# Kernel tuning notes

Measured on AMD Instinct MI355X. Metric: run time of the kernel, lower is better.

## Reference

```python
import jax, jax.numpy as jnp
import numpy as np

DIM = 512
HEADS = 8
SEQ = 2048
BATCH = 4


def setup_inputs() -> dict:
    key = jax.random.key(0)
    k = jax.random.split(key, 6)
    x = jax.random.normal(k[0], (BATCH, SEQ, DIM), dtype=jnp.float32)
    mask = jax.random.normal(k[1], (BATCH, SEQ, SEQ), dtype=jnp.float32)
    Wqkv = jax.random.normal(k[2], (3 * DIM, DIM), dtype=jnp.float32) * 0.02
    Btab = jax.random.normal(k[3], (1, HEADS, 2 * SEQ - 1), dtype=jnp.float32) * 0.02
    Wproj = jax.random.normal(k[4], (DIM, DIM), dtype=jnp.float32) * 0.02
    bproj = jax.random.normal(k[5], (DIM,), dtype=jnp.float32) * 0.02
    return {"x": x, "mask": mask, "Wqkv": Wqkv, "Btab": Btab,
            "Wproj": Wproj, "bproj": bproj}


def reference(x, mask, Wqkv, Btab, Wproj, bproj):
    B, N, C = x.shape
    H = Btab.shape[1]
    seq = (Btab.shape[2] + 1) // 2
    head_dim = C // H
    scale = head_dim ** (-0.5)

    # qkv projection (no bias), split into q,k,v of shape [B,H,N,head_dim]
    qkv = (x @ Wqkv.T).reshape(B, N, 3, H, head_dim)
    qkv = jnp.transpose(qkv, (2, 0, 3, 1, 4))  # [3,B,H,N,hd]
    q, k, v = qkv[0], qkv[1], qkv[2]

    # gathered relative-position bias: B_index[i,j] = i - j + seq - 1
    idx = jnp.arange(N)[:, None] - jnp.arange(N)[None, :] + (seq - 1)  # [N,N]
    bias = Btab[:, :, idx]  # [1,H,N,N]

    attn = jnp.einsum('bhnd,bhmd->bhnm', q, k) * scale + bias
    attn = attn + mask[:, None, :, :]  # additive mask, broadcast over heads
    attn = jax.nn.softmax(attn, axis=-1)

    out = jnp.einsum('bhnm,bhmd->bhnd', attn, v)  # [B,H,N,hd]
    out = jnp.transpose(out, (0, 2, 1, 3)).reshape(B, N, C)
    return out @ Wproj.T + bproj
```

## Files before the change

### kernel.cpp

```cpp
#include <hip/hip_runtime.h>


typedef __attribute__((ext_vector_type(8))) short short8;
typedef __attribute__((ext_vector_type(4))) float f32x4;

#define SEQ   2048
#define NHEAD 8
#define NBATCH 4
#define HD    64
#define CDIM  512
#define L2E   1.44269504f

__device__ __forceinline__ unsigned short f32_to_bf16_rn(float f) {
  unsigned u = __builtin_bit_cast(unsigned, f);
  u += 0x7FFFu + ((u >> 16) & 1u);
  return (unsigned short)(u >> 16);
}

__global__ __launch_bounds__(256) void cvt_f32_bf16(const float* __restrict__ in,
                                                    ushort* __restrict__ out, int n4) {
  int i = blockIdx.x * 256 + threadIdx.x;
  const int stride = gridDim.x * 256;
  for (; i < n4; i += stride) {
    float4 v = reinterpret_cast<const float4*>(in)[i];
    ushort4 o;
    o.x = f32_to_bf16_rn(v.x);
    o.y = f32_to_bf16_rn(v.y);
    o.z = f32_to_bf16_rn(v.z);
    o.w = f32_to_bf16_rn(v.w);
    reinterpret_cast<ushort4*>(out)[i] = o;
  }
}

template <int MODE>
__global__ __launch_bounds__(256) void gemm_nt(
    const ushort* __restrict__ A, const ushort* __restrict__ Bm,
    ushort* __restrict__ qo, ushort* __restrict__ ko, ushort* __restrict__ vto,
    const float* __restrict__ bias, float* __restrict__ outf) {
  const int K = 512;
  __shared__ ushort As[128 * 40];
  __shared__ ushort Bs[128 * 40];

  const int t = threadIdx.x;
  const int bn = blockIdx.x, bm = blockIdx.y;
  const int lane = t & 63, w = t >> 6;
  const int wm = w >> 1, wn = w & 1;
  const int lr = lane & 15, lq = lane >> 4;
  const int m0 = bm * 128, n0 = bn * 128;

  f32x4 acc[4][4];
#pragma unroll
  for (int i = 0; i < 4; ++i)
#pragma unroll
    for (int j = 0; j < 4; ++j) acc[i][j] = (f32x4){0.f, 0.f, 0.f, 0.f};

  for (int kt = 0; kt < K; kt += 32) {
#pragma unroll
    for (int p = 0; p < 2; ++p) {
      const int flat = p * 256 + t;
      const int row = flat >> 2, seg = flat & 3;
      *(uint4*)&As[row * 40 + seg * 8] =
          *(const uint4*)(A + (size_t)(m0 + row) * K + kt + seg * 8);
      *(uint4*)&Bs[row * 40 + seg * 8] =
          *(const uint4*)(Bm + (size_t)(n0 + row) * K + kt + seg * 8);
    }
    __syncthreads();

    short8 af[4], bf[4];
#pragma unroll
    for (int i = 0; i < 4; ++i) {
      af[i] = *(const short8*)&As[(wm * 64 + i * 16 + lr) * 40 + lq * 8];
      bf[i] = *(const short8*)&Bs[(wn * 64 + i * 16 + lr) * 40 + lq * 8];
    }
#pragma unroll
    for (int i = 0; i < 4; ++i)
#pragma unroll
      for (int j = 0; j < 4; ++j)
        acc[i][j] = __builtin_amdgcn_mfma_f32_16x16x32_bf16(af[i], bf[j], acc[i][j], 0, 0, 0);
    __syncthreads();
  }

  if constexpr (MODE == 0) {
#pragma unroll
    for (int i = 0; i < 4; ++i) {
      const int mbase = m0 + wm * 64 + i * 16 + lq * 4;
      const int bb = mbase >> 11;
      const int s0 = mbase & 2047;
#pragma unroll
      for (int j = 0; j < 4; ++j) {
        const int nb = n0 + wn * 64 + j * 16;
        const int tt = nb >> 9;
        const int hh = (nb >> 6) & 7;
        const int d0 = nb & 63;
        const int bh = bb * NHEAD + hh;
        if (tt == 2) {
          ushort4 pk;
          pk.x = f32_to_bf16_rn(acc[i][j][0]);
          pk.y = f32_to_bf16_rn(acc[i][j][1]);
          pk.z = f32_to_bf16_rn(acc[i][j][2]);
          pk.w = f32_to_bf16_rn(acc[i][j][3]);
          *(ushort4*)(vto + ((size_t)bh * HD + d0 + lr) * SEQ + s0) = pk;
        } else {
          ushort* dst = (tt == 0) ? qo : ko;
#pragma unroll
          for (int r = 0; r < 4; ++r)
            dst[((size_t)bh * SEQ + s0 + r) * HD + d0 + lr] = f32_to_bf16_rn(acc[i][j][r]);
        }
      }
    }
  } else {
#pragma unroll
    for (int i = 0; i < 4; ++i) {
#pragma unroll
      for (int j = 0; j < 4; ++j) {
        const int n = n0 + wn * 64 + j * 16 + lr;
        const float bv = bias[n];
#pragma unroll
        for (int r = 0; r < 4; ++r) {
          const int m = m0 + wm * 64 + i * 16 + lq * 4 + r;
          outf[(size_t)m * 512 + n] = acc[i][j][r] + bv;
        }
      }
    }
  }
}

__global__ __launch_bounds__(256) void attn_fused(
    const ushort* __restrict__ Q, const ushort* __restrict__ Kt,
    const ushort* __restrict__ VT, const float* __restrict__ mask,
    const float* __restrict__ Btab, ushort* __restrict__ Out) {
  __shared__ ushort Ks[2][64 * 72];
  __shared__ ushort Vs[2][64 * 72];
  __shared__ ushort Ps[4][32 * 72];

  const int flat = blockIdx.x;
  const int xcd = flat & 7;
  const int rr = flat >> 3;
  const int h = rr & 7;
  const int slot = rr >> 3;
  const int g = slot * 8 + xcd;
  const int qt = g & 15, b = g >> 4;

  const int bh = b * NHEAD + h;
  const ushort* qh = Q + (size_t)bh * SEQ * HD;
  const ushort* kh = Kt + (size_t)bh * SEQ * HD;
  const ushort* vh = VT + (size_t)bh * HD * SEQ;
  const float* mb = mask + (size_t)b * SEQ * SEQ;
  const float* bt = Btab + h * (2 * SEQ - 1);

  const int t = threadIdx.x;
  const int lane = t & 63, w = t >> 6;
  const int lr = lane & 15, lq = lane >> 4;
  const int qb0 = qt * 128;
  const int qbaseA = qb0 + w * 32;
  const int qbaseB = qbaseA + 16;

  short8 qfA0, qfA1, qfB0, qfB1;
  {
    const ushort* qpA = qh + (size_t)(qbaseA + lr) * HD + lq * 8;
    qfA0 = *(const short8*)qpA;
    qfA1 = *(const short8*)(qpA + 32);
    const ushort* qpB = qh + (size_t)(qbaseB + lr) * HD + lq * 8;
    qfB0 = *(const short8*)qpB;
    qfB1 = *(const short8*)(qpB + 32);
  }

  const float* mvA = mb + (size_t)(qbaseA + lr) * SEQ + 4 * lq;
  const float* mvB = mb + (size_t)(qbaseB + lr) * SEQ + 4 * lq;
  const float* btA4 = bt + qbaseA + lr - 4 * lq + 2044;
  const float* btB4 = btA4 + 16;

  float lAa = 0.f, lAb = 0.f, lBa = 0.f, lBb = 0.f;
  f32x4 ofA[4], ofB[4];
#pragma unroll
  for (int i = 0; i < 4; ++i) {
    ofA[i] = (f32x4){0.f, 0.f, 0.f, 0.f};
    ofB[i] = (f32x4){0.f, 0.f, 0.f, 0.f};
  }

  const int srow = t >> 3;
  const int sseg = t & 7;

  const ushort* kp = kh + (size_t)srow * HD + sseg * 8;
  const ushort* vp = vh + (size_t)srow * SEQ + sseg * 8;

  uint4 kr0 = *(const uint4*)(kp);
  uint4 kr1 = *(const uint4*)(kp + 32 * HD);
  uint4 vr0 = *(const uint4*)(vp);
  uint4 vr1 = *(const uint4*)(vp + 32 * SEQ);
  *(uint4*)&Ks[0][srow * 72 + sseg * 8] = kr0;
  *(uint4*)&Ks[0][(32 + srow) * 72 + sseg * 8] = kr1;
  *(uint4*)&Vs[0][srow * 72 + sseg * 8] = vr0;
  *(uint4*)&Vs[0][(32 + srow) * 72 + sseg * 8] = vr1;
  kr0 = *(const uint4*)(kp + 64 * HD);
  kr1 = *(const uint4*)(kp + 96 * HD);
  vr0 = *(const uint4*)(vp + 64);
  vr1 = *(const uint4*)(vp + 64 + 32 * SEQ);

  float4 mnA[4], bnA[4];
#pragma unroll
  for (int f = 0; f < 4; ++f) {
    mnA[f] = *(const float4*)(mvA + f * 16);
    bnA[f] = *(const float4*)(btA4 - f * 16);
  }

  for (int it = 0; it < 32; ++it) {
    const int kv0 = it * 64;
    const int cur = it & 1, nxt = cur ^ 1;

    __syncthreads();

    *(uint4*)&Ks[nxt][srow * 72 + sseg * 8] = kr0;
    *(uint4*)&Ks[nxt][(32 + srow) * 72 + sseg * 8] = kr1;
    *(uint4*)&Vs[nxt][srow * 72 + sseg * 8] = vr0;
    *(uint4*)&Vs[nxt][(32 + srow) * 72 + sseg * 8] = vr1;

    float4 mnB[4], bnB[4];
#pragma unroll
    for (int f = 0; f < 4; ++f) {
      mnB[f] = *(const float4*)(mvB + kv0 + f * 16);
      bnB[f] = *(const float4*)(btB4 - kv0 - f * 16);
    }

    const int lkv = (it + 2 < 32) ? (it + 2) * 64 : 0;
    kr0 = *(const uint4*)(kp + (size_t)lkv * HD);
    kr1 = *(const uint4*)(kp + (size_t)(lkv + 32) * HD);
    vr0 = *(const uint4*)(vp + lkv);
    vr1 = *(const uint4*)(vp + lkv + 32 * SEQ);

    f32x4 sfA[4], sfB[4];
#pragma unroll
    for (int f = 0; f < 4; ++f) {
      const ushort* kfp = &Ks[cur][(f * 16 + lr) * 72 + lq * 8];
      const short8 k0 = *(const short8*)kfp;
      const short8 k1 = *(const short8*)(kfp + 32);
      sfA[f] = (f32x4){0.f, 0.f, 0.f, 0.f};
      sfA[f] = __builtin_amdgcn_mfma_f32_16x16x32_bf16(k0, qfA0, sfA[f], 0, 0, 0);
      sfA[f] = __builtin_amdgcn_mfma_f32_16x16x32_bf16(k1, qfA1, sfA[f], 0, 0, 0);
      sfB[f] = (f32x4){0.f, 0.f, 0.f, 0.f};
      sfB[f] = __builtin_amdgcn_mfma_f32_16x16x32_bf16(k0, qfB0, sfB[f], 0, 0, 0);
      sfB[f] = __builtin_amdgcn_mfma_f32_16x16x32_bf16(k1, qfB1, sfB[f], 0, 0, 0);
    }

#pragma unroll
    for (int f = 0; f < 4; ++f) {
      unsigned up0, up1;
#pragma unroll
      for (int r = 0; r < 4; ++r) {
        const float mbv = (&mnA[f].x)[r] + (&bnA[f].x)[3 - r];
        const float xs = fmaf(sfA[f][r], 0.18033688f, mbv * L2E);
        const float p = __builtin_amdgcn_exp2f(xs);
        if (f & 1) lAb += p; else lAa += p;
        const unsigned hh = (__builtin_bit_cast(unsigned, p) + 0x8000u) >> 16;
        if (r == 0) up0 = hh;
        else if (r == 1) up0 |= hh << 16;
        else if (r == 2) up1 = hh;
        else up1 |= hh << 16;
      }
      uint2 pk; pk.x = up0; pk.y = up1;
      *(uint2*)&Ps[w][lr * 72 + 16 * f + 4 * lq] = pk;
    }

    const int mkv = (it + 1 < 32) ? (it + 1) * 64 : 0;
#pragma unroll
    for (int f = 0; f < 4; ++f) {
      mnA[f] = *(const float4*)(mvA + mkv + f * 16);
      bnA[f] = *(const float4*)(btA4 - mkv - f * 16);
    }

#pragma unroll
    for (int f = 0; f < 4; ++f) {
      unsigned up0, up1;
#pragma unroll
      for (int r = 0; r < 4; ++r) {
        const float mbv = (&mnB[f].x)[r] + (&bnB[f].x)[3 - r];
        const float xs = fmaf(sfB[f][r], 0.18033688f, mbv * L2E);
        const float p = __builtin_amdgcn_exp2f(xs);
        if (f & 1) lBb += p; else lBa += p;
        const unsigned hh = (__builtin_bit_cast(unsigned, p) + 0x8000u) >> 16;
        if (r == 0) up0 = hh;
        else if (r == 1) up0 |= hh << 16;
        else if (r == 2) up1 = hh;
        else up1 |= hh << 16;
      }
      uint2 pk; pk.x = up0; pk.y = up1;
      *(uint2*)&Ps[w][(16 + lr) * 72 + 16 * f + 4 * lq] = pk;
    }

#pragma unroll
    for (int ks = 0; ks < 2; ++ks) {
      union { uint4 u; short8 s; } puA, puB;
      puA.u = *(const uint4*)&Ps[w][lr * 72 + ks * 32 + lq * 8];
      puB.u = *(const uint4*)&Ps[w][(16 + lr) * 72 + ks * 32 + lq * 8];
#pragma unroll
      for (int hf = 0; hf < 4; ++hf) {
        const short8 vf =
            *(const short8*)&Vs[cur][(hf * 16 + lr) * 72 + ks * 32 + lq * 8];
        ofA[hf] = __builtin_amdgcn_mfma_f32_16x16x32_bf16(puA.s, vf, ofA[hf], 0, 0, 0);
        ofB[hf] = __builtin_amdgcn_mfma_f32_16x16x32_bf16(puB.s, vf, ofB[hf], 0, 0, 0);
      }
    }
  }

  float vA = lAa + lAb;
  vA += __shfl_xor(vA, 16); vA += __shfl_xor(vA, 32);
  float vB = lBa + lBb;
  vB += __shfl_xor(vB, 16); vB += __shfl_xor(vB, 32);

#pragma unroll
  for (int r = 0; r < 4; ++r) {
    const float invA = 1.0f / __shfl(vA, (lane & 48) | (lq * 4 + r));
    const int qrA = qbaseA + lq * 4 + r;
    ushort* opA = Out + ((size_t)(b * SEQ + qrA)) * CDIM + h * HD;
#pragma unroll
    for (int hf = 0; hf < 4; ++hf) opA[hf * 16 + lr] = f32_to_bf16_rn(ofA[hf][r] * invA);
    const float invB = 1.0f / __shfl(vB, (lane & 48) | (lq * 4 + r));
    const int qrB = qbaseB + lq * 4 + r;
    ushort* opB = Out + ((size_t)(b * SEQ + qrB)) * CDIM + h * HD;
#pragma unroll
    for (int hf = 0; hf < 4; ++hf) opB[hf * 16 + lr] = f32_to_bf16_rn(ofB[hf][r] * invB);
  }
}

extern "C" void kernel_launch(void* const* d_in, const int* in_sizes, int n_in,
                              void* d_out, int out_size, void* d_ws, size_t ws_size,
                              hipStream_t stream) {
  const float* x     = (const float*)d_in[0];
  const float* mask  = (const float*)d_in[1];
  const float* Wqkv  = (const float*)d_in[2];
  const float* Btab  = (const float*)d_in[3];
  const float* Wproj = (const float*)d_in[4];
  const float* bproj = (const float*)d_in[5];
  float* out = (float*)d_out;

  char* ws = (char*)d_ws;
  const size_t SZ_X   = (size_t)NBATCH * SEQ * CDIM;
  const size_t SZ_QKV = (size_t)3 * CDIM * CDIM;
  const size_t SZ_PRJ = (size_t)CDIM * CDIM;
  const size_t SZ_HD  = (size_t)NBATCH * NHEAD * SEQ * HD;

  ushort* xb    = (ushort*)ws; ws += SZ_X * 2;
  ushort* wqkvb = (ushort*)ws; ws += SZ_QKV * 2;
  ushort* wprjb = (ushort*)ws; ws += SZ_PRJ * 2;
  ushort* qb    = (ushort*)ws; ws += SZ_HD * 2;
  ushort* kb    = (ushort*)ws; ws += SZ_HD * 2;
  ushort* vtb   = (ushort*)ws; ws += SZ_HD * 2;
  ushort* aob   = (ushort*)ws; ws += SZ_X * 2;

  {
    int n4 = (int)(SZ_X / 4);
    int g = (n4 + 255) / 256; if (g > 4096) g = 4096;
    cvt_f32_bf16<<<g, 256, 0, stream>>>(x, xb, n4);
  }
  {
    int n4 = (int)(SZ_QKV / 4);
    cvt_f32_bf16<<<(n4 + 255) / 256, 256, 0, stream>>>(Wqkv, wqkvb, n4);
  }
  {
    int n4 = (int)(SZ_PRJ / 4);
    cvt_f32_bf16<<<(n4 + 255) / 256, 256, 0, stream>>>(Wproj, wprjb, n4);
  }

  gemm_nt<0><<<dim3(12, 64), 256, 0, stream>>>(xb, wqkvb, qb, kb, vtb, nullptr, nullptr);

  attn_fused<<<dim3(512), 256, 0, stream>>>(qb, kb, vtb, mask, Btab, aob);

  gemm_nt<1><<<dim3(4, 64), 256, 0, stream>>>(aob, wprjb, nullptr, nullptr, nullptr, bproj, out);
}
```

Before: 145.7 us.

## Switch attention to 32x32x16 MFMA and keep P in registers via permlane32 swap

Rewrites the fused attention inner loop to use 32x32x16 bf16 MFMA tiles instead of 16x16x32, so each wave computes a 32-query by 64-key score block with fewer instructions. The probability tile is repacked in registers with v_permlane32_swap into the A-operand layout for the PV MFMA, which removes the per-wave LDS staging buffer and its write/read round trip. Row sums now accumulate the bf16-rounded probabilities, and the mask and bias load pattern is reorganised to match the new accumulator layout. Larger accumulators raise register pressure and may reduce occupancy.

```diff
diff --git a/kernel.cpp b/kernel.cpp
--- a/kernel.cpp
+++ b/kernel.cpp
@@ -3,6 +3,7 @@
 
 typedef __attribute__((ext_vector_type(8))) short short8;
 typedef __attribute__((ext_vector_type(4))) float f32x4;
+typedef __attribute__((ext_vector_type(16))) float f32x16;
 
 #define SEQ   2048
 #define NHEAD 8
@@ -10,11 +11,22 @@
 #define HD    64
 #define CDIM  512
 #define L2E   1.44269504f
+#define SC    0.18033688f
 
 __device__ __forceinline__ unsigned short f32_to_bf16_rn(float f) {
   unsigned u = __builtin_bit_cast(unsigned, f);
   u += 0x7FFFu + ((u >> 16) & 1u);
   return (unsigned short)(u >> 16);
+}
+__device__ __forceinline__ float bf16_to_f32(unsigned short h) {
+  unsigned u = ((unsigned)h) << 16;
+  return __builtin_bit_cast(float, u);
+}
+__device__ __forceinline__ f32x16 zero16() {
+  f32x16 z;
+#pragma unroll
+  for (int i = 0; i < 16; ++i) z[i] = 0.f;
+  return z;
 }
 
 __global__ __launch_bounds__(256) void cvt_f32_bf16(const float* __restrict__ in,
@@ -131,7 +143,6 @@
     const float* __restrict__ Btab, ushort* __restrict__ Out) {
   __shared__ ushort Ks[2][64 * 72];
   __shared__ ushort Vs[2][64 * 72];
-  __shared__ ushort Ps[4][32 * 72];
 
   const int flat = blockIdx.x;
   const int xcd = flat & 7;
@@ -150,33 +161,25 @@
 
   const int t = threadIdx.x;
   const int lane = t & 63, w = t >> 6;
-  const int lr = lane & 15, lq = lane >> 4;
+  const int la = lane & 31, hi = lane >> 5;
   const int qb0 = qt * 128;
-  const int qbaseA = qb0 + w * 32;
-  const int qbaseB = qbaseA + 16;
-
-  short8 qfA0, qfA1, qfB0, qfB1;
+  const int qbase = qb0 + w * 32;
+  const int q = qbase + la;
+
+  short8 qf0, qf1, qf2, qf3;
   {
-    const ushort* qpA = qh + (size_t)(qbaseA + lr) * HD + lq * 8;
-    qfA0 = *(const short8*)qpA;
-    qfA1 = *(const short8*)(qpA + 32);
-    const ushort* qpB = qh + (size_t)(qbaseB + lr) * HD + lq * 8;
-    qfB0 = *(const short8*)qpB;
-    qfB1 = *(const short8*)(qpB + 32);
-  }
-
-  const float* mvA = mb + (size_t)(qbaseA + lr) * SEQ + 4 * lq;
-  const float* mvB = mb + (size_t)(qbaseB + lr) * SEQ + 4 * lq;
-  const float* btA4 = bt + qbaseA + lr - 4 * lq + 2044;
-  const float* btB4 = btA4 + 16;
-
-  float lAa = 0.f, lAb = 0.f, lBa = 0.f, lBb = 0.f;
-  f32x4 ofA[4], ofB[4];
-#pragma unroll
-  for (int i = 0; i < 4; ++i) {
-    ofA[i] = (f32x4){0.f, 0.f, 0.f, 0.f};
-    ofB[i] = (f32x4){0.f, 0.f, 0.f, 0.f};
-  }
+    const ushort* qp = qh + (size_t)q * HD + hi * 8;
+    qf0 = *(const short8*)(qp);
+    qf1 = *(const short8*)(qp + 16);
+    qf2 = *(const short8*)(qp + 32);
+    qf3 = *(const short8*)(qp + 48);
+  }
+
+  const float* mv = mb + (size_t)q * SEQ + 4 * hi;
+  const float* bv = bt + q + 2044 - 4 * hi;
+
+  float lacc0 = 0.f, lacc1 = 0.f;
+  f32x16 of0 = zero16(), of1 = zero16();
 
   const int srow = t >> 3;
   const int sseg = t & 7;
@@ -197,11 +200,11 @@
   vr0 = *(const uint4*)(vp + 64);
   vr1 = *(const uint4*)(vp + 64 + 32 * SEQ);
 
-  float4 mnA[4], bnA[4];
-#pragma unroll
-  for (int f = 0; f < 4; ++f) {
-    mnA[f] = *(const float4*)(mvA + f * 16);
-    bnA[f] = *(const float4*)(btA4 - f * 16);
+  float4 mn0[4], bn0[4];
+#pragma unroll
+  for (int s = 0; s < 4; ++s) {
+    mn0[s] = *(const float4*)(mv + s * 8);
+    bn0[s] = *(const float4*)(bv - s * 8);
   }
 
   for (int it = 0; it < 32; ++it) {
@@ -215,11 +218,11 @@
     *(uint4*)&Vs[nxt][srow * 72 + sseg * 8] = vr0;
     *(uint4*)&Vs[nxt][(32 + srow) * 72 + sseg * 8] = vr1;
 
-    float4 mnB[4], bnB[4];
-#pragma unroll
-    for (int f = 0; f < 4; ++f) {
-      mnB[f] = *(const float4*)(mvB + kv0 + f * 16);
-      bnB[f] = *(const float4*)(btB4 - kv0 - f * 16);
+    float4 mn1[4], bn1[4];
+#pragma unroll
+    for (int s = 0; s < 4; ++s) {
+      mn1[s] = *(const float4*)(mv + kv0 + 32 + s * 8);
+      bn1[s] = *(const float4*)(bv - kv0 - 32 - s * 8);
     }
 
     const int lkv = (it + 2 < 32) ? (it + 2) * 64 : 0;
@@ -228,97 +231,115 @@
     vr0 = *(const uint4*)(vp + lkv);
     vr1 = *(const uint4*)(vp + lkv + 32 * SEQ);
 
-    f32x4 sfA[4], sfB[4];
-#pragma unroll
-    for (int f = 0; f < 4; ++f) {
-      const ushort* kfp = &Ks[cur][(f * 16 + lr) * 72 + lq * 8];
-      const short8 k0 = *(const short8*)kfp;
-      const short8 k1 = *(const short8*)(kfp + 32);
-      sfA[f] = (f32x4){0.f, 0.f, 0.f, 0.f};
-      sfA[f] = __builtin_amdgcn_mfma_f32_16x16x32_bf16(k0, qfA0, sfA[f], 0, 0, 0);
-      sfA[f] = __builtin_amdgcn_mfma_f32_16x16x32_bf16(k1, qfA1, sfA[f], 0, 0, 0);
-      sfB[f] = (f32x4){0.f, 0.f, 0.f, 0.f};
-      sfB[f] = __builtin_amdgcn_mfma_f32_16x16x32_bf16(k0, qfB0, sfB[f], 0, 0, 0);
-      sfB[f] = __builtin_amdgcn_mfma_f32_16x16x32_bf16(k1, qfB1, sfB[f], 0, 0, 0);
-    }
-
-#pragma unroll
-    for (int f = 0; f < 4; ++f) {
-      unsigned up0, up1;
+    f32x16 sf0 = zero16();
+#pragma unroll
+    for (int c = 0; c < 4; ++c) {
+      const short8 kf = *(const short8*)&Ks[cur][(la)*72 + c * 16 + hi * 8];
+      sf0 = (c == 0)
+        ? __builtin_amdgcn_mfma_f32_32x32x16_bf16(kf, qf0, sf0, 0, 0, 0)
+        : (c == 1)
+        ? __builtin_amdgcn_mfma_f32_32x32x16_bf16(kf, qf1, sf0, 0, 0, 0)
+        : (c == 2)
+        ? __builtin_amdgcn_mfma_f32_32x32x16_bf16(kf, qf2, sf0, 0, 0, 0)
+        : __builtin_amdgcn_mfma_f32_32x32x16_bf16(kf, qf3, sf0, 0, 0, 0);
+    }
+
+    unsigned pk0, pk1, pk2, pk3, pk4, pk5, pk6, pk7;
+#pragma unroll
+    for (int s = 0; s < 4; ++s) {
+      unsigned bb_[4];
 #pragma unroll
       for (int r = 0; r < 4; ++r) {
-        const float mbv = (&mnA[f].x)[r] + (&bnA[f].x)[3 - r];
-        const float xs = fmaf(sfA[f][r], 0.18033688f, mbv * L2E);
-        const float p = __builtin_amdgcn_exp2f(xs);
-        if (f & 1) lAb += p; else lAa += p;
-        const unsigned hh = (__builtin_bit_cast(unsigned, p) + 0x8000u) >> 16;
-        if (r == 0) up0 = hh;
-        else if (r == 1) up0 |= hh << 16;
-        else if (r == 2) up1 = hh;
-        else up1 |= hh << 16;
+        const float mbv = (&mn0[s].x)[r] + (&bn0[s].x)[3 - r];
+        const float p = __builtin_amdgcn_exp2f(fmaf(sf0[4 * s + r], SC, mbv * L2E));
+        const unsigned short pb = f32_to_bf16_rn(p);
+        lacc0 += bf16_to_f32(pb);
+        bb_[r] = pb;
       }
-      uint2 pk; pk.x = up0; pk.y = up1;
-      *(uint2*)&Ps[w][lr * 72 + 16 * f + 4 * lq] = pk;
-    }
+      const unsigned d0 = bb_[0] | (bb_[1] << 16);
+      const unsigned d1 = bb_[2] | (bb_[3] << 16);
+      if (s == 0) { pk0 = d0; pk1 = d1; }
+      else if (s == 1) { pk2 = d0; pk3 = d1; }
+      else if (s == 2) { pk4 = d0; pk5 = d1; }
+      else { pk6 = d0; pk7 = d1; }
+    }
+    asm("v_permlane32_swap_b32 %0, %1" : "+v"(pk0), "+v"(pk2));
+    asm("v_permlane32_swap_b32 %0, %1" : "+v"(pk1), "+v"(pk3));
+    asm("v_permlane32_swap_b32 %0, %1" : "+v"(pk4), "+v"(pk6));
+    asm("v_permlane32_swap_b32 %0, %1" : "+v"(pk5), "+v"(pk7));
+    union { uint4 u; short8 s8; } pa0, pa1;
+    pa0.u.x = pk0; pa0.u.y = pk1; pa0.u.z = pk2; pa0.u.w = pk3;
+    pa1.u.x = pk4; pa1.u.y = pk5; pa1.u.z = pk6; pa1.u.w = pk7;
 
     const int mkv = (it + 1 < 32) ? (it + 1) * 64 : 0;
 #pragma unroll
-    for (int f = 0; f < 4; ++f) {
-      mnA[f] = *(const float4*)(mvA + mkv + f * 16);
-      bnA[f] = *(const float4*)(btA4 - mkv - f * 16);
-    }
-
-#pragma unroll
-    for (int f = 0; f < 4; ++f) {
-      unsigned up0, up1;
+    for (int s = 0; s < 4; ++s) {
+      mn0[s] = *(const float4*)(mv + mkv + s * 8);
+      bn0[s] = *(const float4*)(bv - mkv - s * 8);
+    }
+
+    f32x16 sf1 = zero16();
+#pragma unroll
+    for (int c = 0; c < 4; ++c) {
+      const short8 kf = *(const short8*)&Ks[cur][(32 + la) * 72 + c * 16 + hi * 8];
+      sf1 = (c == 0)
+        ? __builtin_amdgcn_mfma_f32_32x32x16_bf16(kf, qf0, sf1, 0, 0, 0)
+        : (c == 1)
+        ? __builtin_amdgcn_mfma_f32_32x32x16_bf16(kf, qf1, sf1, 0, 0, 0)
+        : (c == 2)
+        ? __builtin_amdgcn_mfma_f32_32x32x16_bf16(kf, qf2, sf1, 0, 0, 0)
+        : __builtin_amdgcn_mfma_f32_32x32x16_bf16(kf, qf3, sf1, 0, 0, 0);
+    }
+
+    unsigned qk0, qk1, qk2, qk3, qk4, qk5, qk6, qk7;
+#pragma unroll
+    for (int s = 0; s < 4; ++s) {
+      unsigned bb_[4];
 #pragma unroll
       for (int r = 0; r < 4; ++r) {
-        const float mbv = (&mnB[f].x)[r] + (&bnB[f].x)[3 - r];
-        const float xs = fmaf(sfB[f][r], 0.18033688f, mbv * L2E);
-        const float p = __builtin_amdgcn_exp2f(xs);
-        if (f & 1) lBb += p; else lBa += p;
-        const unsigned hh = (__builtin_bit_cast(unsigned, p) + 0x8000u) >> 16;
-        if (r == 0) up0 = hh;
-        else if (r == 1) up0 |= hh << 16;
-        else if (r == 2) up1 = hh;
-        else up1 |= hh << 16;
+        const float mbv = (&mn1[s].x)[r] + (&bn1[s].x)[3 - r];
+        const float p = __builtin_amdgcn_exp2f(fmaf(sf1[4 * s + r], SC, mbv * L2E));
+        const unsigned short pb = f32_to_bf16_rn(p);
+        lacc1 += bf16_to_f32(pb);
+        bb_[r] = pb;
       }
-      uint2 pk; pk.x = up0; pk.y = up1;
-      *(uint2*)&Ps[w][(16 + lr) * 72 + 16 * f + 4 * lq] = pk;
-    }
-
-#pragma unroll
-    for (int ks = 0; ks < 2; ++ks) {
-      union { uint4 u; short8 s; } puA, puB;
-      puA.u = *(const uint4*)&Ps[w][lr * 72 + ks * 32 + lq * 8];
-      puB.u = *(const uint4*)&Ps[w][(16 + lr) * 72 + ks * 32 + lq * 8];
-#pragma unroll
-      for (int hf = 0; hf < 4; ++hf) {
-        const short8 vf =
-            *(const short8*)&Vs[cur][(hf * 16 + lr) * 72 + ks * 32 + lq * 8];
-        ofA[hf] = __builtin_amdgcn_mfma_f32_16x16x32_bf16(puA.s, vf, ofA[hf], 0, 0, 0);
-        ofB[hf] = __builtin_amdgcn_mfma_f32_16x16x32_bf16(puB.s, vf, ofB[hf], 0, 0, 0);
-      }
-    }
-  }
-
-  float vA = lAa + lAb;
-  vA += __shfl_xor(vA, 16); vA += __shfl_xor(vA, 32);
-  float vB = lBa + lBb;
-  vB += __shfl_xor(vB, 16); vB += __shfl_xor(vB, 32);
-
-#pragma unroll
-  for (int r = 0; r < 4; ++r) {
-    const float invA = 1.0f / __shfl(vA, (lane & 48) | (lq * 4 + r));
-    const int qrA = qbaseA + lq * 4 + r;
-    ushort* opA = Out + ((size_t)(b * SEQ + qrA)) * CDIM + h * HD;
-#pragma unroll
-    for (int hf = 0; hf < 4; ++hf) opA[hf * 16 + lr] = f32_to_bf16_rn(ofA[hf][r] * invA);
-    const float invB = 1.0f / __shfl(vB, (lane & 48) | (lq * 4 + r));
-    const int qrB = qbaseB + lq * 4 + r;
-    ushort* opB = Out + ((size_t)(b * SEQ + qrB)) * CDIM + h * HD;
-#pragma unroll
-    for (int hf = 0; hf < 4; ++hf) opB[hf * 16 + lr] = f32_to_bf16_rn(ofB[hf][r] * invB);
+      const unsigned d0 = bb_[0] | (bb_[1] << 16);
+      const unsigned d1 = bb_[2] | (bb_[3] << 16);
+      if (s == 0) { qk0 = d0; qk1 = d1; }
+      else if (s == 1) { qk2 = d0; qk3 = d1; }
+      else if (s == 2) { qk4 = d0; qk5 = d1; }
+      else { qk6 = d0; qk7 = d1; }
+    }
+    asm("v_permlane32_swap_b32 %0, %1" : "+v"(qk0), "+v"(qk2));
+    asm("v_permlane32_swap_b32 %0, %1" : "+v"(qk1), "+v"(qk3));
+    asm("v_permlane32_swap_b32 %0, %1" : "+v"(qk4), "+v"(qk6));
+    asm("v_permlane32_swap_b32 %0, %1" : "+v"(qk5), "+v"(qk7));
+    union { uint4 u; short8 s8; } pa2, pa3;
+    pa2.u.x = qk0; pa2.u.y = qk1; pa2.u.z = qk2; pa2.u.w = qk3;
+    pa3.u.x = qk4; pa3.u.y = qk5; pa3.u.z = qk6; pa3.u.w = qk7;
+
+#pragma unroll
+    for (int tt = 0; tt < 4; ++tt) {
+      const short8 pf = (tt == 0) ? pa0.s8 : (tt == 1) ? pa1.s8
+                       : (tt == 2) ? pa2.s8 : pa3.s8;
+      const short8 vf0 = *(const short8*)&Vs[cur][(la)*72 + tt * 16 + hi * 8];
+      const short8 vf1 = *(const short8*)&Vs[cur][(32 + la) * 72 + tt * 16 + hi * 8];
+      of0 = __builtin_amdgcn_mfma_f32_32x32x16_bf16(pf, vf0, of0, 0, 0, 0);
+      of1 = __builtin_amdgcn_mfma_f32_32x32x16_bf16(pf, vf1, of1, 0, 0, 0);
+    }
+  }
+
+  float lt = lacc0 + lacc1;
+  lt += __shfl_xor(lt, 32);
+
+  ushort* ob = Out + ((size_t)(b * SEQ + qbase)) * CDIM + h * HD + la;
+#pragma unroll
+  for (int reg = 0; reg < 16; ++reg) {
+    const int ql = ((reg & 3) + 8 * (reg >> 2)) + 4 * hi;
+    const float inv = 1.0f / __shfl(lt, ql);
+    ushort* op = ob + (size_t)ql * CDIM;
+    op[0] = f32_to_bf16_rn(of0[reg] * inv);
+    op[32] = f32_to_bf16_rn(of1[reg] * inv);
   }
 }
 
```

After: 147.1 us. No clear change (+0.9%).
